# Performance work log

Measured on AMD Instinct MI355X. Metric: run time of the kernel, lower is better.

## Reference

```python
import jax, jax.numpy as jnp
import numpy as np

EPS = 1e-3  # keras BatchNormalization default epsilon


def _conv1x1(x, W, b):
    # x: (b, h, w, cin), W: (cin, cout)
    return jnp.einsum('bhwc,cd->bhwd', x, W) + b


def _bn(x, gamma, beta, mean, var):
    # inference-mode batch norm (moving statistics)
    return gamma * (x - mean) * jax.lax.rsqrt(var + EPS) + beta


def setup_inputs() -> dict:
    key = jax.random.key(0)
    ks = jax.random.split(key, 20)
    C, Ci = 512, 256
    B, Ha, Wa, Hd, Wd = 8, 32, 32, 64, 64
    s_in = 1.0 / np.sqrt(C)
    s_ic = 1.0 / np.sqrt(Ci)
    inp = {
        'detect': jax.random.normal(ks[0], (B, Hd, Wd, C), jnp.float32),
        'aim': jax.random.normal(ks[1], (B, Ha, Wa, C), jnp.float32),
        # g, theta, phi: C -> Ci 1x1 convs
        'Wg': jax.random.normal(ks[2], (C, Ci), jnp.float32) * s_in,
        'bg': jnp.zeros((Ci,), jnp.float32),
        'Wt': jax.random.normal(ks[3], (C, Ci), jnp.float32) * s_in,
        'bt': jnp.zeros((Ci,), jnp.float32),
        'Wp': jax.random.normal(ks[4], (C, Ci), jnp.float32) * s_in,
        'bp': jnp.zeros((Ci,), jnp.float32),
        # W branch: Ci -> C conv + BN
        'Ww': jax.random.normal(ks[5], (Ci, C), jnp.float32) * s_ic,
        'bw': jnp.zeros((C,), jnp.float32),
        'gw': jnp.ones((C,), jnp.float32),
        'betw': jnp.zeros((C,), jnp.float32),
        'mw': jax.random.normal(ks[6], (C,), jnp.float32) * 0.1,
        'vw': jax.random.uniform(ks[7], (C,), jnp.float32, 0.5, 1.5),
        # Q branch: Ci -> C conv + BN
        'Wq': jax.random.normal(ks[8], (Ci, C), jnp.float32) * s_ic,
        'bq': jnp.zeros((C,), jnp.float32),
        'gq': jnp.ones((C,), jnp.float32),
        'betq': jnp.zeros((C,), jnp.float32),
        'mq': jax.random.normal(ks[9], (C,), jnp.float32) * 0.1,
        'vq': jax.random.uniform(ks[10], (C,), jnp.float32, 0.5, 1.5),
    }
    return inp


def reference(detect, aim, Wg, bg, Wt, bt, Wp, bp,
              Ww, bw, gw, betw, mw, vw,
              Wq, bq, gq, betq, mq, vq):
    B, Ha, Wa, C = aim.shape
    _, Hd, Wd, _ = detect.shape
    Ci = Wg.shape[1]
    Na, Nd = Ha * Wa, Hd * Wd

    d_x = _conv1x1(detect, Wg, bg).reshape(B, Nd, Ci)     # (b, Nd, Ci)
    a_x = _conv1x1(aim, Wg, bg).reshape(B, Na, Ci)        # (b, Na, Ci)
    theta_x = _conv1x1(aim, Wt, bt).reshape(B, Na, Ci)    # (b, Na, Ci)
    phi_x = _conv1x1(detect, Wp, bp).reshape(B, Nd, Ci)   # (b, Nd, Ci)

    # affinity: (b, Na, Nd)
    f = jnp.einsum('bnc,bmc->bnm', theta_x, phi_x)
    f_div_C = f / Nd          # normalize by last dim of f
    fi_div_C = jnp.swapaxes(f, 1, 2) / Na  # (b, Nd, Na), normalized by its last dim

    non_aim = jnp.einsum('bnm,bmc->bnc', f_div_C, d_x).reshape(B, Ha, Wa, Ci)
    non_aim = _bn(_conv1x1(non_aim, Ww, bw), gw, betw, mw, vw) + aim

    non_det = jnp.einsum('bmn,bnc->bmc', fi_div_C, a_x).reshape(B, Hd, Wd, Ci)
    non_det = _bn(_conv1x1(non_det, Wq, bq), gq, betq, mq, vq) + detect

    return non_aim, non_det
```

## Files before the change

### kernel.cpp

```cpp
#include <hip/hip_runtime.h>

typedef unsigned short ushort_t;
typedef unsigned int uint32;
typedef __bf16 bf16x8 __attribute__((ext_vector_type(8)));
typedef float f32x4 __attribute__((ext_vector_type(4)));
typedef uint32 u32x4 __attribute__((ext_vector_type(4)));
typedef uint32 u32x2 __attribute__((ext_vector_type(2)));

typedef __attribute__((address_space(3))) uint32 as3_u32;
typedef const __attribute__((address_space(1))) uint32 as1_u32c;

__device__ __forceinline__ void gl_lds16(const ushort_t* g, ushort_t* l) {
    __builtin_amdgcn_global_load_lds((as1_u32c*)g, (as3_u32*)l, 16, 0, 0);
}

__device__ __forceinline__ float bf2f(ushort_t u) {
    uint32 x = ((uint32)u) << 16;
    return __builtin_bit_cast(float, x);
}
__device__ __forceinline__ ushort_t f2bf(float f) {
    uint32 x = __builtin_bit_cast(uint32, f);
    x += 0x7fffu + ((x >> 16) & 1u);
    return (ushort_t)(x >> 16);
}
__device__ __forceinline__ void ld4bf(const ushort_t* p, float* f) {
    const u32x2 w = *(const u32x2*)p;
    f[0] = bf2f((ushort_t)(w[0] & 0xffffu)); f[1] = bf2f((ushort_t)(w[0] >> 16));
    f[2] = bf2f((ushort_t)(w[1] & 0xffffu)); f[3] = bf2f((ushort_t)(w[1] >> 16));
}
__device__ __forceinline__ u32x2 pk4bf(const float* v) {
    u32x2 pk;
    pk[0] = (uint32)f2bf(v[0]) | ((uint32)f2bf(v[1]) << 16);
    pk[1] = (uint32)f2bf(v[2]) | ((uint32)f2bf(v[3]) << 16);
    return pk;
}

__device__ __forceinline__ bool sniff(const void* in0) {
    const uint32* s = (const uint32*)in0;
    const int lane = threadIdx.x & 63;
    int wd = 0;
    for (int c = 0; c < 4; c++) {
        const uint32 w = s[lane * 4 + c];
        const uint32 e = (w >> 7) & 0xFFu;
        wd += (e < 64u) || (e >= 192u);
    }
    for (int off = 32; off; off >>= 1) wd += __shfl_down(wd, off);
    return __shfl(wd, 0) > 32;
}

struct VecArgs { const void* s[14]; ushort_t* d[14]; int n[14]; };
struct WtArgs { const void* s[6]; ushort_t* d[6]; int R[6]; int C[6]; };
__global__ void canon_all(const void* __restrict__ dsrc, ushort_t* __restrict__ ddst,
                          const void* __restrict__ asrc, ushort_t* __restrict__ adst,
                          WtArgs wa, VecArgs va, int* __restrict__ flag) {
    const bool isf32 = sniff(dsrc);
    const int b = blockIdx.x;
    if (b < 3072) {
        const void* src; ushort_t* dst; long n; int b0, nb;
        if (b < 2560) { src = dsrc; dst = ddst; n = 16777216; b0 = b; nb = 2560; }
        else          { src = asrc; dst = adst; n = 4194304;  b0 = b - 2560; nb = 512; }
        long i = ((long)b0 * 256 + threadIdx.x) * 16;
        const long stride = (long)nb * 256 * 16;
        if (isf32) {
            const float* s = (const float*)src;
            for (; i < n; i += stride) {
                const f32x4 a0 = *(const f32x4*)(s + i);
                const f32x4 a1 = *(const f32x4*)(s + i + 4);
                const f32x4 a2 = *(const f32x4*)(s + i + 8);
                const f32x4 a3 = *(const f32x4*)(s + i + 12);
                u32x4 o0, o1;
                o0[0] = (uint32)f2bf(a0[0]) | ((uint32)f2bf(a0[1]) << 16);
                o0[1] = (uint32)f2bf(a0[2]) | ((uint32)f2bf(a0[3]) << 16);
                o0[2] = (uint32)f2bf(a1[0]) | ((uint32)f2bf(a1[1]) << 16);
                o0[3] = (uint32)f2bf(a1[2]) | ((uint32)f2bf(a1[3]) << 16);
                o1[0] = (uint32)f2bf(a2[0]) | ((uint32)f2bf(a2[1]) << 16);
                o1[1] = (uint32)f2bf(a2[2]) | ((uint32)f2bf(a2[3]) << 16);
                o1[2] = (uint32)f2bf(a3[0]) | ((uint32)f2bf(a3[1]) << 16);
                o1[3] = (uint32)f2bf(a3[2]) | ((uint32)f2bf(a3[3]) << 16);
                *(u32x4*)(dst + i) = o0;
                *(u32x4*)(dst + i + 8) = o1;
            }
        } else {
            const ushort_t* s = (const ushort_t*)src;
            for (; i < n; i += stride) {
                const u32x4 v0 = *(const u32x4*)(s + i);
                const u32x4 v1 = *(const u32x4*)(s + i + 8);
                *(u32x4*)(dst + i) = v0;
                *(u32x4*)(dst + i + 8) = v1;
            }
        }
    } else if (b < 4608) {
        const int local = b - 3072;
        const int wsel = local >> 8;
        const int rem = local & 255;
        const int tr = rem >> 4, tc = rem & 15;
        const int R = wa.R[wsel], C = wa.C[wsel];
        if (tc * 32 >= C || tr * 32 >= R) return;
        __shared__ float s[32][33];
        const int t = threadIdx.x;
        const int r = t >> 3, c4 = (t & 7) * 4;
        const long sbase = (long)(tr * 32 + r) * C + tc * 32 + c4;
        if (isf32) {
            const float* S = (const float*)wa.s[wsel];
            const f32x4 v = *(const f32x4*)(S + sbase);
            for (int u = 0; u < 4; u++) s[r][c4 + u] = v[u];
        } else {
            const ushort_t* S = (const ushort_t*)wa.s[wsel];
            for (int u = 0; u < 4; u++) s[r][c4 + u] = bf2f(S[sbase + u]);
        }
        __syncthreads();
        float tv[4];
        for (int u = 0; u < 4; u++) tv[u] = s[c4 + u][r];
        *(u32x2*)(wa.d[wsel] + (long)(tc * 32 + r) * R + tr * 32 + c4) = pk4bf(tv);
    } else {
        if (threadIdx.x == 0) *flag = isf32 ? 1 : 0;
        const int t = threadIdx.x;
        for (int seg = 0; seg < 14; seg++) {
            const int n = va.n[seg];
            if (isf32) {
                const float* s = (const float*)va.s[seg];
                for (int i = t; i < n; i += 256) va.d[seg][i] = f2bf(s[i]);
            } else {
                const ushort_t* s = (const ushort_t*)va.s[seg];
                for (int i = t; i < n; i += 256) va.d[seg][i] = s[i];
            }
        }
    }
}

__global__ void reduce_g_kernel(const float* __restrict__ P1, const float* __restrict__ P2,
                                ushort_t* __restrict__ G1, ushort_t* __restrict__ G2) {
    const int bxv = blockIdx.x;
    const int zz = bxv >> 6;
    const float* P = (zz < 8) ? P1 : P2;
    ushort_t* G    = (zz < 8) ? G1 : G2;
    const float alpha = (zz < 8) ? (1.f / 4096.f) : (1.f / 1024.f);
    const int b = zz & 7;
    const long off = ((long)(bxv & 63) * 256 + threadIdx.x) * 4;
    const float* base = P + (long)b * 16 * 65536 + off;
    f32x4 acc = {0.f, 0.f, 0.f, 0.f};
    for (int kc = 0; kc < 16; kc++) acc += *(const f32x4*)(base + (long)kc * 65536);
    float v[4] = {acc[0] * alpha, acc[1] * alpha, acc[2] * alpha, acc[3] * alpha};
    *(u32x2*)(G + (long)b * 65536 + off) = pk4bf(v);
}

#define BM 128
#define BN 128
#define BK 32
#define LDSH (BM * BK)
#define NBUF 3
#define BIGN (1 << 30)

enum { EPI_BIAS = 0, EPI_BIASR = 1, EPI_SCALE = 2, EPI_BN = 3, EPI_PART = 4 };

struct GP {
    const ushort_t* A; const ushort_t* B; void* Cv; ushort_t* CT;
    const ushort_t* bias; const ushort_t* gamma; const ushort_t* beta;
    const ushort_t* mean; const ushort_t* var; const ushort_t* res;
    long coff, sA, sB, sC;
    int K, lda, ldb, ldc, cnmax, ldT, bshift;
    float alpha;
};
struct GP2 { GP g[2]; };

template <int EPI, bool DYNOUT, bool DUALT, bool SWAP>
__global__ __launch_bounds__(256) void gemm_nt(GP2 ga, int ysplit, int zsplit,
                                               const int* __restrict__ flag)
{
    __shared__ __align__(16) ushort_t As[NBUF * LDSH];
    __shared__ __align__(16) ushort_t Bs[NBUF * LDSH];

    const bool isf32 = DYNOUT ? (*flag != 0) : false;

    const uint32 gx = gridDim.x, gy = gridDim.y;
    const uint32 nwg = gx * gy * gridDim.z;
    const uint32 lid = blockIdx.x + gx * (blockIdx.y + gy * blockIdx.z);
    const uint32 swz = (lid & 7u) * (nwg >> 3) + (lid >> 3);
    const uint32 bx = swz % gx, t1 = swz / gx;
    int by = (int)(t1 % gy), bz = (int)(t1 / gy);

    int sel = 0;
    if (by >= ysplit) { by -= ysplit; sel = 1; }
    if (bz >= zsplit) { bz -= zsplit; sel = 1; }
    const GP& p = ga.g[sel];

    const ushort_t* A = p.A + (long)bz * p.sA;
    const ushort_t* B = p.B + ((long)bz + (long)(by >> p.bshift)) * p.sB;
    const long cbase = p.coff + (long)bz * p.sC;
    const int lda = p.lda, ldb = p.ldb, ldc = p.ldc, K = p.K;

    const int tid  = threadIdx.x;
    const int lane = tid & 63;
    const int w    = tid >> 6;
    const int wr   = w >> 1, wc = w & 1;
    const int lr   = lane & 15, q = lane >> 4;

    const int m0 = by * BM;
    const int n0 = bx * BN;

    const int lrow = lane >> 2, lu = lane & 3;
    const int us = (lu ^ ((lrow >> 1) & 3)) * 8;
    const int ra0 = w * 32 + lrow, ra1 = w * 32 + 16 + lrow;
    const ushort_t* Ar0 = A + (long)(m0 + ra0) * lda + us;
    const ushort_t* Ar1 = A + (long)(m0 + ra1) * lda + us;
    const ushort_t* Br0 = B + (long)(n0 + ra0) * ldb + us;
    const ushort_t* Br1 = B + (long)(n0 + ra1) * ldb + us;
    ushort_t* sA0 = &As[(w * 2 + 0) * 512];
    ushort_t* sA1 = &As[(w * 2 + 1) * 512];
    ushort_t* sB0 = &Bs[(w * 2 + 0) * 512];
    ushort_t* sB1 = &Bs[(w * 2 + 1) * 512];

    const int swq = (q ^ ((lr >> 1) & 3)) * 8;

    f32x4 acc[4][4];
#pragma unroll
    for (int i = 0; i < 4; i++)
#pragma unroll
        for (int j = 0; j < 4; j++) acc[i][j] = (f32x4){0.f, 0.f, 0.f, 0.f};

    const int nt = K / BK;
    {
        gl_lds16(Ar0, sA0); gl_lds16(Ar1, sA1);
        gl_lds16(Br0, sB0); gl_lds16(Br1, sB1);
        if (nt > 1) {
            gl_lds16(Ar0 + BK, sA0 + LDSH); gl_lds16(Ar1 + BK, sA1 + LDSH);
            gl_lds16(Br0 + BK, sB0 + LDSH); gl_lds16(Br1 + BK, sB1 + LDSH);
        }
    }

    int c0 = 0, c2 = 2;
    for (int t = 0; t < nt; ++t) {
        if (t + 1 < nt) asm volatile("s_waitcnt vmcnt(4)" ::: "memory");
        else            asm volatile("s_waitcnt vmcnt(0)" ::: "memory");
        __builtin_amdgcn_s_barrier();
        __builtin_amdgcn_sched_barrier(0);

        if (t + 2 < nt) {
            const int nb = c2 * LDSH;
            const int kn = (t + 2) * BK;
            gl_lds16(Ar0 + kn, sA0 + nb); gl_lds16(Ar1 + kn, sA1 + nb);
            gl_lds16(Br0 + kn, sB0 + nb); gl_lds16(Br1 + kn, sB1 + nb);
        }
        __builtin_amdgcn_sched_barrier(0);

        const ushort_t* Ab = As + c0 * LDSH;
        const ushort_t* Bb = Bs + c0 * LDSH;
        bf16x8 af[4], bfr[4];
#pragma unroll
        for (int i = 0; i < 4; i++)
            af[i] = __builtin_bit_cast(bf16x8,
                *(const u32x4*)(&Ab[(wr * 64 + i * 16 + lr) * BK + swq]));
#pragma unroll
        for (int j = 0; j < 4; j++)
            bfr[j] = __builtin_bit_cast(bf16x8,
                *(const u32x4*)(&Bb[(wc * 64 + j * 16 + lr) * BK + swq]));
#pragma unroll
        for (int i = 0; i < 4; i++)
#pragma unroll
            for (int j = 0; j < 4; j++) {
                if constexpr (SWAP)
                    acc[i][j] = __builtin_amdgcn_mfma_f32_16x16x32_bf16(bfr[j], af[i], acc[i][j], 0, 0, 0);
                else
                    acc[i][j] = __builtin_amdgcn_mfma_f32_16x16x32_bf16(af[i], bfr[j], acc[i][j], 0, 0, 0);
            }
        __builtin_amdgcn_sched_barrier(0);

        c0 = (c0 + 1 == NBUF) ? 0 : c0 + 1;
        c2 = (c2 + 1 == NBUF) ? 0 : c2 + 1;
    }

    if constexpr (SWAP) {
#pragma unroll
        for (int j = 0; j < 4; j++) {
            const int coln = n0 + wc * 64 + j * 16 + q * 4;
            float sc4[4], sh4[4];
            if constexpr (EPI == EPI_BIAS) {
                float bb[4]; ld4bf(p.bias + coln, bb);
#pragma unroll
                for (int r = 0; r < 4; r++) { sc4[r] = 1.f; sh4[r] = bb[r]; }
            } else if constexpr (EPI == EPI_SCALE) {
#pragma unroll
                for (int r = 0; r < 4; r++) { sc4[r] = p.alpha; sh4[r] = 0.f; }
            } else if constexpr (EPI == EPI_BN) {
                float bb[4], g[4], bt[4], mn[4], vr[4];
                ld4bf(p.bias + coln, bb); ld4bf(p.gamma + coln, g); ld4bf(p.beta + coln, bt);
                ld4bf(p.mean + coln, mn); ld4bf(p.var + coln, vr);
#pragma unroll
                for (int r = 0; r < 4; r++) {
                    const float s = g[r] * rsqrtf(vr[r] + 1e-3f);
                    sc4[r] = s;
                    sh4[r] = s * bb[r] + bt[r] - s * mn[r];
                }
            }
#pragma unroll
            for (int i = 0; i < 4; i++) {
                const int row = m0 + wr * 64 + i * 16 + lr;
                const long off = cbase + (long)row * ldc + coln;
                float v[4];
#pragma unroll
                for (int r = 0; r < 4; r++) v[r] = acc[i][j][r];
                if constexpr (EPI == EPI_BIASR) {
                    const float bs = bf2f(p.bias[row]);
#pragma unroll
                    for (int r = 0; r < 4; r++) v[r] += bs;
                } else if constexpr (EPI == EPI_BN) {
                    float rs[4]; ld4bf(p.res + (long)row * ldc + coln, rs);
#pragma unroll
                    for (int r = 0; r < 4; r++) v[r] = sc4[r] * v[r] + sh4[r] + rs[r];
                } else if constexpr (EPI != EPI_PART) {
#pragma unroll
                    for (int r = 0; r < 4; r++) v[r] = sc4[r] * v[r] + sh4[r];
                }
                if constexpr (EPI == EPI_PART) {
                    *(f32x4*)((float*)p.Cv + off) = (f32x4){v[0], v[1], v[2], v[3]};
                } else if constexpr (DYNOUT) {
                    if (isf32) *(f32x4*)((float*)p.Cv + off) = (f32x4){v[0], v[1], v[2], v[3]};
                    else       *(u32x2*)((ushort_t*)p.Cv + off) = pk4bf(v);
                } else {
                    *(u32x2*)((ushort_t*)p.Cv + off) = pk4bf(v);
                }
            }
        }
    } else {
        const bool doC = (n0 < p.cnmax);
#pragma unroll
        for (int j = 0; j < 4; j++) {
            const int col = n0 + wc * 64 + j * 16 + lr;
            float bs = 0.f;
            if constexpr (EPI == EPI_BIAS) bs = bf2f(p.bias[col]);
#pragma unroll
            for (int i = 0; i < 4; i++) {
                const int rowbase = m0 + wr * 64 + i * 16 + q * 4;
                ushort_t tmp[4];
#pragma unroll
                for (int r = 0; r < 4; r++) {
                    const int row = rowbase + r;
                    float v = acc[i][j][r];
                    if constexpr (EPI == EPI_BIAS) v += bs;
                    else if constexpr (EPI == EPI_BIASR) v += bf2f(p.bias[row]);
                    else if constexpr (EPI == EPI_SCALE) v *= p.alpha;
                    const long off = cbase + (long)row * ldc + col;
                    if constexpr (EPI == EPI_PART) {
                        ((float*)p.Cv)[off] = v;
                    } else {
                        const ushort_t us2 = f2bf(v);
                        tmp[r] = us2;
                        if (doC) ((ushort_t*)p.Cv)[off] = us2;
                    }
                }
                if constexpr (DUALT) {
                    u32x2 pk;
                    pk[0] = (uint32)tmp[0] | ((uint32)tmp[1] << 16);
                    pk[1] = (uint32)tmp[2] | ((uint32)tmp[3] << 16);
                    *(u32x2*)(p.CT + (long)bz * p.sC + (long)col * p.ldT + rowbase) = pk;
                }
            }
        }
    }
}

extern "C" void kernel_launch(void* const* d_in, const int* in_sizes, int n_in,
                              void* d_out, int out_size, void* d_ws, size_t ws_size,
                              hipStream_t stream)
{
    int* flag = (int*)d_ws;
    ushort_t* base = (ushort_t*)((char*)d_ws + 512);
    long o = 0;
    ushort_t* detect_c = base + o; o += 16777216;
    ushort_t* aim_c    = base + o; o += 4194304;
    ushort_t* WpgT = base + o; o += 262144;
    ushort_t* WtgT = base + o; o += 262144;
    ushort_t* WwT  = base + o; o += 131072;
    ushort_t* WqT  = base + o; o += 131072;
    ushort_t* bpg_c  = base + o; o += 512;
    ushort_t* btg_c  = base + o; o += 512;
    ushort_t* bw_c   = base + o; o += 512;
    ushort_t* gw_c   = base + o; o += 512;
    ushort_t* betw_c = base + o; o += 512;
    ushort_t* mw_c   = base + o; o += 512;
    ushort_t* vw_c   = base + o; o += 512;
    ushort_t* bq_c   = base + o; o += 512;
    ushort_t* gq_c   = base + o; o += 512;
    ushort_t* betq_c = base + o; o += 512;
    ushort_t* mq_c   = base + o; o += 512;
    ushort_t* vq_c   = base + o; o += 512;
    ushort_t* phi    = base + o; o += 8388608;
    ushort_t* PT     = base + o; o += 16777216;
    ushort_t* theta  = base + o; o += 2097152;
    ushort_t* TT     = base + o; o += 4194304;
    ushort_t* G1     = base + o; o += 524288;
    ushort_t* G2     = base + o; o += 524288;
    ushort_t* M1T    = base + o; o += 1048576;
    ushort_t* M2T    = base + o; o += 1048576;
    ushort_t* U      = base + o; o += 33554432;
    float* P1 = (float*)U;
    float* P2 = P1 + 8388608;
    ushort_t* phiT = PT;
    ushort_t* d_xT = PT + 8388608;
    ushort_t* thetaT = TT;
    ushort_t* a_xT = TT + 2097152;

    VecArgs va;
    const int vidx[14] = {7, 3, 5, 3, 9, 10, 11, 12, 13, 15, 16, 17, 18, 19};
    ushort_t* vdst[14] = {bpg_c, bpg_c + 256, btg_c, btg_c + 256,
                          bw_c, gw_c, betw_c, mw_c, vw_c,
                          bq_c, gq_c, betq_c, mq_c, vq_c};
    const int vn[14] = {256, 256, 256, 256, 512, 512, 512, 512, 512, 512, 512, 512, 512, 512};
    for (int i = 0; i < 14; i++) { va.s[i] = d_in[vidx[i]]; va.d[i] = vdst[i]; va.n[i] = vn[i]; }

    WtArgs wa;
    wa.s[0] = d_in[6];  wa.d[0] = WpgT;              wa.R[0] = 512; wa.C[0] = 256;
    wa.s[1] = d_in[2];  wa.d[1] = WpgT + 256 * 512;  wa.R[1] = 512; wa.C[1] = 256;
    wa.s[2] = d_in[4];  wa.d[2] = WtgT;              wa.R[2] = 512; wa.C[2] = 256;
    wa.s[3] = d_in[2];  wa.d[3] = WtgT + 256 * 512;  wa.R[3] = 512; wa.C[3] = 256;
    wa.s[4] = d_in[8];  wa.d[4] = WwT;               wa.R[4] = 256; wa.C[4] = 512;
    wa.s[5] = d_in[14]; wa.d[5] = WqT;               wa.R[5] = 256; wa.C[5] = 512;

    canon_all<<<4609, 256, 0, stream>>>(d_in[0], detect_c, d_in[1], aim_c, wa, va, flag);

    const dim3 blk(256);
    const ushort_t* np = nullptr;
    ushort_t* npm = nullptr;

    {
        GP2 g;
        g.g[0] = GP{detect_c, WpgT, phi, PT, bpg_c, np, np, np, np, np,
                    0, 0, 0, 0, 512, 512, 512, 256, 256, 32768, 30, 1.f};
        g.g[1] = GP{aim_c, WtgT, theta, TT, btg_c, np, np, np, np, np,
                    0, 0, 0, 0, 512, 512, 512, 256, 256, 8192, 30, 1.f};
        gemm_nt<EPI_BIAS, false, true, false><<<dim3(4, 320, 1), blk, 0, stream>>>(
            g, 256, BIGN, flag);
    }

    {
        GP2 g;
        g.g[0] = GP{phiT, d_xT, P1, npm, np, np, np, np, np, np,
                    0, 256, 256, 65536, 256, 32768, 32768, 256, BIGN, 0, 30, 1.f};
        g.g[1] = GP{thetaT, a_xT, P2, npm, np, np, np, np, np, np,
                    0, 64, 64, 65536, 64, 8192, 8192, 256, BIGN, 0, 30, 1.f};
        gemm_nt<EPI_PART, false, false, true><<<dim3(2, 2, 256), blk, 0, stream>>>(
            g, BIGN, 128, flag);
    }

    reduce_g_kernel<<<1024, blk, 0, stream>>>(P1, P2, G1, G2);

    {
        GP2 g;
        g.g[0] = GP{G1, WwT, npm, M1T, np, np, np, np, np, np,
                    0, 65536, 0, 131072, 256, 256, 256, 512, 0, 256, 30, 1.f};
        g.g[1] = GP{G2, WqT, npm, M2T, np, np, np, np, np, np,
                    0, 65536, 0, 131072, 256, 256, 256, 512, 0, 256, 30, 1.f};
        gemm_nt<EPI_SCALE, false, true, false><<<dim3(4, 2, 16), blk, 0, stream>>>(
            g, BIGN, 8, flag);
    }

    {
        GP2 g;
        g.g[0] = GP{phi, M2T, d_out, npm, bq_c, gq_c, betq_c, mq_c, vq_c, detect_c,
                    8192L * 512, 0, 131072, 0, 256, 256, 256, 512, BIGN, 0, 5, 1.f};
        g.g[1] = GP{theta, M1T, d_out, npm, bw_c, gw_c, betw_c, mw_c, vw_c, aim_c,
                    0, 0, 131072, 0, 256, 256, 256, 512, BIGN, 0, 3, 1.f};
        gemm_nt<EPI_BN, true, false, true><<<dim3(4, 320, 1), blk, 0, stream>>>(
            g, 256, BIGN, flag);
    }
}
```

Baseline: 329.5 us.

## Add 64-row tile GEMM variant for projection and BN output GEMMs

Introduces a gemm_nt64 kernel with 64xBN tiles, each of the four waves owning a 32-column slice, and simple double buffering. The first projection GEMM and the final BN-epilogue GEMM now use it with twice as many workgroups, and bshift is adjusted to the new row tiling. The SWAP epilogue in the original gemm_nt is stripped of its bias/BN/scale handling because the remaining users (EPI_PART) don't need it. Smaller tiles are meant to improve occupancy and load balance, at the cost of lower operand reuse per tile and more redundant weight loads.

```diff
diff --git a/kernel.cpp b/kernel.cpp
--- a/kernel.cpp
+++ b/kernel.cpp
@@ -273,25 +273,6 @@
 #pragma unroll
         for (int j = 0; j < 4; j++) {
             const int coln = n0 + wc * 64 + j * 16 + q * 4;
-            float sc4[4], sh4[4];
-            if constexpr (EPI == EPI_BIAS) {
-                float bb[4]; ld4bf(p.bias + coln, bb);
-#pragma unroll
-                for (int r = 0; r < 4; r++) { sc4[r] = 1.f; sh4[r] = bb[r]; }
-            } else if constexpr (EPI == EPI_SCALE) {
-#pragma unroll
-                for (int r = 0; r < 4; r++) { sc4[r] = p.alpha; sh4[r] = 0.f; }
-            } else if constexpr (EPI == EPI_BN) {
-                float bb[4], g[4], bt[4], mn[4], vr[4];
-                ld4bf(p.bias + coln, bb); ld4bf(p.gamma + coln, g); ld4bf(p.beta + coln, bt);
-                ld4bf(p.mean + coln, mn); ld4bf(p.var + coln, vr);
-#pragma unroll
-                for (int r = 0; r < 4; r++) {
-                    const float s = g[r] * rsqrtf(vr[r] + 1e-3f);
-                    sc4[r] = s;
-                    sh4[r] = s * bb[r] + bt[r] - s * mn[r];
-                }
-            }
 #pragma unroll
             for (int i = 0; i < 4; i++) {
                 const int row = m0 + wr * 64 + i * 16 + lr;
@@ -299,18 +280,6 @@
                 float v[4];
 #pragma unroll
                 for (int r = 0; r < 4; r++) v[r] = acc[i][j][r];
-                if constexpr (EPI == EPI_BIASR) {
-                    const float bs = bf2f(p.bias[row]);
-#pragma unroll
-                    for (int r = 0; r < 4; r++) v[r] += bs;
-                } else if constexpr (EPI == EPI_BN) {
-                    float rs[4]; ld4bf(p.res + (long)row * ldc + coln, rs);
-#pragma unroll
-                    for (int r = 0; r < 4; r++) v[r] = sc4[r] * v[r] + sh4[r] + rs[r];
-                } else if constexpr (EPI != EPI_PART) {
-#pragma unroll
-                    for (int r = 0; r < 4; r++) v[r] = sc4[r] * v[r] + sh4[r];
-                }
                 if constexpr (EPI == EPI_PART) {
                     *(f32x4*)((float*)p.Cv + off) = (f32x4){v[0], v[1], v[2], v[3]};
                 } else if constexpr (DYNOUT) {
@@ -353,6 +322,182 @@
                     pk[0] = (uint32)tmp[0] | ((uint32)tmp[1] << 16);
                     pk[1] = (uint32)tmp[2] | ((uint32)tmp[3] << 16);
                     *(u32x2*)(p.CT + (long)bz * p.sC + (long)col * p.ldT + rowbase) = pk;
+                }
+            }
+        }
+    }
+}
+
+#define LDSA64 (64 * 32)
+#define LDSB64 (128 * 32)
+template <int EPI, bool DYNOUT, bool DUALT, bool SWAP>
+__global__ __launch_bounds__(256) void gemm_nt64(GP2 ga, int ysplit,
+                                                 const int* __restrict__ flag)
+{
+    __shared__ __align__(16) ushort_t As[2 * LDSA64];
+    __shared__ __align__(16) ushort_t Bs[2 * LDSB64];
+
+    const bool isf32 = DYNOUT ? (*flag != 0) : false;
+
+    const uint32 gx = gridDim.x, gy = gridDim.y;
+    const uint32 nwg = gx * gy;
+    const uint32 lid = blockIdx.x + gx * blockIdx.y;
+    const uint32 swz = (lid & 7u) * (nwg >> 3) + (lid >> 3);
+    const uint32 bx = swz % gx;
+    int by = (int)(swz / gx);
+
+    int sel = 0;
+    if (by >= ysplit) { by -= ysplit; sel = 1; }
+    const GP& p = ga.g[sel];
+
+    const ushort_t* A = p.A;
+    const ushort_t* B = p.B + (long)(by >> p.bshift) * p.sB;
+    const long cbase = p.coff;
+    const int lda = p.lda, ldb = p.ldb, ldc = p.ldc, K = p.K;
+
+    const int tid  = threadIdx.x;
+    const int lane = tid & 63;
+    const int w    = tid >> 6;
+    const int wc   = w;
+    const int lr   = lane & 15, q = lane >> 4;
+
+    const int m0 = by * 64;
+    const int n0 = bx * BN;
+
+    const int lrow = lane >> 2, lu = lane & 3;
+    const int us = (lu ^ ((lrow >> 1) & 3)) * 8;
+    const ushort_t* ArS = A + (long)(m0 + w * 16 + lrow) * lda + us;
+    const ushort_t* Br0 = B + (long)(n0 + w * 32 + lrow) * ldb + us;
+    const ushort_t* Br1 = B + (long)(n0 + w * 32 + 16 + lrow) * ldb + us;
+    ushort_t* sAw = &As[w * 512];
+    ushort_t* sB0 = &Bs[(w * 2 + 0) * 512];
+    ushort_t* sB1 = &Bs[(w * 2 + 1) * 512];
+
+    const int swq = (q ^ ((lr >> 1) & 3)) * 8;
+
+    f32x4 acc[4][2];
+#pragma unroll
+    for (int i = 0; i < 4; i++)
+#pragma unroll
+        for (int j = 0; j < 2; j++) acc[i][j] = (f32x4){0.f, 0.f, 0.f, 0.f};
+
+    const int nt = K / BK;
+    gl_lds16(ArS, sAw);
+    gl_lds16(Br0, sB0);
+    gl_lds16(Br1, sB1);
+
+    for (int t = 0; t < nt; ++t) {
+        const int cur = t & 1;
+        if (t + 1 < nt) {
+            const int kn = (t + 1) * BK;
+            const int nbA = (cur ^ 1) * LDSA64, nbB = (cur ^ 1) * LDSB64;
+            gl_lds16(ArS + kn, sAw + nbA);
+            gl_lds16(Br0 + kn, sB0 + nbB);
+            gl_lds16(Br1 + kn, sB1 + nbB);
+            asm volatile("s_waitcnt vmcnt(3)" ::: "memory");
+        } else {
+            asm volatile("s_waitcnt vmcnt(0)" ::: "memory");
+        }
+        __builtin_amdgcn_s_barrier();
+        __builtin_amdgcn_sched_barrier(0);
+
+        const ushort_t* Ab = As + cur * LDSA64;
+        const ushort_t* Bb = Bs + cur * LDSB64;
+        bf16x8 af[4], bfr[2];
+#pragma unroll
+        for (int i = 0; i < 4; i++)
+            af[i] = __builtin_bit_cast(bf16x8,
+                *(const u32x4*)(&Ab[(i * 16 + lr) * BK + swq]));
+#pragma unroll
+        for (int j = 0; j < 2; j++)
+            bfr[j] = __builtin_bit_cast(bf16x8,
+                *(const u32x4*)(&Bb[(wc * 32 + j * 16 + lr) * BK + swq]));
+#pragma unroll
+        for (int i = 0; i < 4; i++)
+#pragma unroll
+            for (int j = 0; j < 2; j++) {
+                if constexpr (SWAP)
+                    acc[i][j] = __builtin_amdgcn_mfma_f32_16x16x32_bf16(bfr[j], af[i], acc[i][j], 0, 0, 0);
+                else
+                    acc[i][j] = __builtin_amdgcn_mfma_f32_16x16x32_bf16(af[i], bfr[j], acc[i][j], 0, 0, 0);
+            }
+        __builtin_amdgcn_sched_barrier(0);
+        asm volatile("" ::: "memory");
+        __builtin_amdgcn_s_barrier();
+    }
+
+    if constexpr (SWAP) {
+#pragma unroll
+        for (int j = 0; j < 2; j++) {
+            const int coln = n0 + wc * 32 + j * 16 + q * 4;
+            float sc4[4], sh4[4];
+            if constexpr (EPI == EPI_BN) {
+                float bb[4], g[4], bt[4], mn[4], vr[4];
+                ld4bf(p.bias + coln, bb); ld4bf(p.gamma + coln, g); ld4bf(p.beta + coln, bt);
+                ld4bf(p.mean + coln, mn); ld4bf(p.var + coln, vr);
+#pragma unroll
+                for (int r = 0; r < 4; r++) {
+                    const float s = g[r] * rsqrtf(vr[r] + 1e-3f);
+                    sc4[r] = s;
+                    sh4[r] = s * bb[r] + bt[r] - s * mn[r];
+                }
+            } else if constexpr (EPI == EPI_BIAS) {
+                float bb[4]; ld4bf(p.bias + coln, bb);
+#pragma unroll
+                for (int r = 0; r < 4; r++) { sc4[r] = 1.f; sh4[r] = bb[r]; }
+            } else {
+#pragma unroll
+                for (int r = 0; r < 4; r++) { sc4[r] = p.alpha; sh4[r] = 0.f; }
+            }
+#pragma unroll
+            for (int i = 0; i < 4; i++) {
+                const int row = m0 + i * 16 + lr;
+                const long off = cbase + (long)row * ldc + coln;
+                float v[4];
+#pragma unroll
+                for (int r = 0; r < 4; r++) v[r] = acc[i][j][r];
+                if constexpr (EPI == EPI_BN) {
+                    float rs[4]; ld4bf(p.res + (long)row * ldc + coln, rs);
+#pragma unroll
+                    for (int r = 0; r < 4; r++) v[r] = sc4[r] * v[r] + sh4[r] + rs[r];
+                } else {
+#pragma unroll
+                    for (int r = 0; r < 4; r++) v[r] = sc4[r] * v[r] + sh4[r];
+                }
+                if constexpr (DYNOUT) {
+                    if (isf32) *(f32x4*)((float*)p.Cv + off) = (f32x4){v[0], v[1], v[2], v[3]};
+                    else       *(u32x2*)((ushort_t*)p.Cv + off) = pk4bf(v);
+                } else {
+                    *(u32x2*)((ushort_t*)p.Cv + off) = pk4bf(v);
+                }
+            }
+        }
+    } else {
+        const bool doC = (n0 < p.cnmax);
+#pragma unroll
+        for (int j = 0; j < 2; j++) {
+            const int col = n0 + wc * 32 + j * 16 + lr;
+            float bs = 0.f;
+            if constexpr (EPI == EPI_BIAS) bs = bf2f(p.bias[col]);
+#pragma unroll
+            for (int i = 0; i < 4; i++) {
+                const int rowbase = m0 + i * 16 + q * 4;
+                ushort_t tmp[4];
+#pragma unroll
+                for (int r = 0; r < 4; r++) {
+                    const int row = rowbase + r;
+                    float v = acc[i][j][r];
+                    if constexpr (EPI == EPI_BIAS) v += bs;
+                    const long off = cbase + (long)row * ldc + col;
+                    const ushort_t us2 = f2bf(v);
+                    tmp[r] = us2;
+                    if (doC) ((ushort_t*)p.Cv)[off] = us2;
+                }
+                if constexpr (DUALT) {
+                    u32x2 pk;
+                    pk[0] = (uint32)tmp[0] | ((uint32)tmp[1] << 16);
+                    pk[1] = (uint32)tmp[2] | ((uint32)tmp[3] << 16);
+                    *(u32x2*)(p.CT + (long)col * p.ldT + rowbase) = pk;
                 }
             }
         }
@@ -428,8 +573,8 @@
                     0, 0, 0, 0, 512, 512, 512, 256, 256, 32768, 30, 1.f};
         g.g[1] = GP{aim_c, WtgT, theta, TT, btg_c, np, np, np, np, np,
                     0, 0, 0, 0, 512, 512, 512, 256, 256, 8192, 30, 1.f};
-        gemm_nt<EPI_BIAS, false, true, false><<<dim3(4, 320, 1), blk, 0, stream>>>(
-            g, 256, BIGN, flag);
+        gemm_nt64<EPI_BIAS, false, true, false><<<dim3(4, 640, 1), blk, 0, stream>>>(
+            g, 512, flag);
     }
 
     {
@@ -457,10 +602,10 @@
     {
         GP2 g;
         g.g[0] = GP{phi, M2T, d_out, npm, bq_c, gq_c, betq_c, mq_c, vq_c, detect_c,
-                    8192L * 512, 0, 131072, 0, 256, 256, 256, 512, BIGN, 0, 5, 1.f};
+                    8192L * 512, 0, 131072, 0, 256, 256, 256, 512, BIGN, 0, 6, 1.f};
         g.g[1] = GP{theta, M1T, d_out, npm, bw_c, gw_c, betw_c, mw_c, vw_c, aim_c,
-                    0, 0, 131072, 0, 256, 256, 256, 512, BIGN, 0, 3, 1.f};
-        gemm_nt<EPI_BN, true, false, true><<<dim3(4, 320, 1), blk, 0, stream>>>(
-            g, 256, BIGN, flag);
-    }
-}
+                    0, 0, 131072, 0, 256, 256, 256, 512, BIGN, 0, 4, 1.f};
+        gemm_nt64<EPI_BN, true, false, true><<<dim3(4, 640, 1), blk, 0, stream>>>(
+            g, 512, flag);
+    }
+}
```

Result: no change. 324.6 us (-1.5%).
